# Performance work log

Measured on AMD Instinct MI355X. Metric: run time of the kernel, lower is better.

## Reference

```python
import jax, jax.numpy as jnp
import numpy as np

N_NODES = 100000
N_EDGES = 3200000
F_IN = 256
N_CLASSES = 10


def setup_inputs() -> dict:
    key = jax.random.key(0)
    ks = jax.random.split(key, 10)
    x = jax.random.normal(ks[0], (N_NODES, F_IN), dtype=jnp.float32)
    edge_index = jax.random.randint(ks[1], (2, N_EDGES), 0, N_NODES, dtype=jnp.int64)
    def glorot(k, fan_in, fan_out):
        s = (6.0 / (fan_in + fan_out)) ** 0.5
        return jax.random.uniform(k, (fan_in, fan_out), jnp.float32, -s, s)
    return {
        "x": x,
        "edge_index": edge_index,
        "W_gcn": glorot(ks[2], F_IN, 64),
        "b_gcn": jnp.zeros((64,), jnp.float32),
        "W1": glorot(ks[3], 64, 32),
        "b1": jnp.zeros((32,), jnp.float32),
        "W2": glorot(ks[4], 32, 16),
        "b2": jnp.zeros((16,), jnp.float32),
        "W3": glorot(ks[5], 16, N_CLASSES),
        "b3": jnp.zeros((N_CLASSES,), jnp.float32),
    }


def gcn_conv(x, edge_index, W, b):
    # PyG GCNConv: x' = D^{-1/2} (A + I) D^{-1/2} (x W) + b, with self-loops.
    n = x.shape[0]
    loop = jnp.arange(n, dtype=edge_index.dtype)
    src = jnp.concatenate([edge_index[0], loop])  # [E+N]
    dst = jnp.concatenate([edge_index[1], loop])
    deg = jax.ops.segment_sum(jnp.ones(src.shape, jnp.float32), dst, num_segments=n)
    dinv = jnp.where(deg > 0, jax.lax.rsqrt(deg), 0.0)
    norm = dinv[src] * dinv[dst]  # [E+N]
    h = x @ W  # transform first (reduces message width to 64)
    msg = h[src] * norm[:, None]  # gather + scale
    out = jax.ops.segment_sum(msg, dst, num_segments=n)  # scatter-add
    return out + b


def reference(x, edge_index, W_gcn, b_gcn, W1, b1, W2, b2, W3, b3):
    # Dropout is a no-op in eval mode; reference uses deterministic eval math.
    h = jax.nn.relu(gcn_conv(x, edge_index, W_gcn, b_gcn))
    h = jax.nn.relu(h @ W1 + b1)
    h = jax.nn.relu(h @ W2 + b2)
    return h @ W3 + b3
```

## Files before the change

### kernel.cpp

```cpp
#include <hip/hip_runtime.h>

#define F_IN 256
#define CHUNK 8192
#define CAP 10240

typedef short bf8_t __attribute__((ext_vector_type(8)));
typedef float f4_t  __attribute__((ext_vector_type(4)));

__device__ __forceinline__ unsigned short f2bf(float f) {
  unsigned u = __float_as_uint(f);
  unsigned r = (u + 0x7FFFu + ((u >> 16) & 1u)) >> 16;
  return (unsigned short)r;
}
#define BF_LO(d) __uint_as_float((d) << 16)
#define BF_HI(d) __uint_as_float((d) & 0xFFFF0000u)

__device__ __forceinline__ bf8_t pack8(float4 a, float4 b) {
  bf8_t r;
  r[0] = (short)f2bf(a.x); r[1] = (short)f2bf(a.y);
  r[2] = (short)f2bf(a.z); r[3] = (short)f2bf(a.w);
  r[4] = (short)f2bf(b.x); r[5] = (short)f2bf(b.y);
  r[6] = (short)f2bf(b.z); r[7] = (short)f2bf(b.w);
  return r;
}

__global__ __launch_bounds__(256) void wprep_kernel(
    const float* __restrict__ W, unsigned short* __restrict__ WbT) {
  const int i = blockIdx.x * 256 + threadIdx.x;
  const int k = i >> 6, n = i & 63;
  WbT[n * 256 + k] = f2bf(W[i]);
}

__global__ __launch_bounds__(256) void gemm_direct_kernel(
    const float* __restrict__ x, const unsigned short* __restrict__ WbT,
    const int* __restrict__ deg, unsigned short* __restrict__ hb, int M) {
  __shared__ short Bs[64][264];
  const int t = threadIdx.x;
  for (int i = t; i < 2048; i += 256) {
    const int n = i >> 5, kq = (i & 31) << 3;
    *(uint4*)&Bs[n][kq] = *(const uint4*)(WbT + n * 256 + kq);
  }
  __syncthreads();

  const int brow = blockIdx.x * 128;
  const int w = t >> 6;
  const int l = t & 63;
  const int ml = l & 15;
  const int quad = l >> 4;

  const int r0 = min(brow + w * 32 + ml, M - 1);
  const int r1 = min(brow + w * 32 + 16 + ml, M - 1);
  const float* xr0 = x + (size_t)r0 * F_IN + (quad << 3);
  const float* xr1 = x + (size_t)r1 * F_IN + (quad << 3);

  f4_t acc[2][4];
#pragma unroll
  for (int a = 0; a < 2; ++a)
#pragma unroll
    for (int b = 0; b < 4; ++b) acc[a][b] = (f4_t){0.f, 0.f, 0.f, 0.f};

#pragma unroll
  for (int k0 = 0; k0 < F_IN; k0 += 32) {
    bf8_t afr[2];
    {
      const float4 a0 = *(const float4*)(xr0 + k0);
      const float4 a1 = *(const float4*)(xr0 + k0 + 4);
      afr[0] = pack8(a0, a1);
      const float4 c0 = *(const float4*)(xr1 + k0);
      const float4 c1 = *(const float4*)(xr1 + k0 + 4);
      afr[1] = pack8(c0, c1);
    }
    bf8_t bfr[4];
#pragma unroll
    for (int nt = 0; nt < 4; ++nt)
      bfr[nt] = *(const bf8_t*)&Bs[nt * 16 + ml][k0 + (quad << 3)];
#pragma unroll
    for (int mt = 0; mt < 2; ++mt)
#pragma unroll
      for (int nt = 0; nt < 4; ++nt)
        acc[mt][nt] = __builtin_amdgcn_mfma_f32_16x16x32_bf16(
            afr[mt], bfr[nt], acc[mt][nt], 0, 0, 0);
  }

#pragma unroll
  for (int mt = 0; mt < 2; ++mt) {
#pragma unroll
    for (int reg = 0; reg < 4; ++reg) {
      const int row = brow + w * 32 + mt * 16 + (quad << 2) + reg;
      if (row < M) {
        const float di = rsqrtf((float)deg[row] + 1.f);
#pragma unroll
        for (int nt = 0; nt < 4; ++nt)
          hb[(size_t)row * 64 + nt * 16 + ml] = f2bf(di * acc[mt][nt][reg]);
      }
    }
  }
}

__global__ __launch_bounds__(512) void sort_local_kernel(
    const int* __restrict__ src_arr, const int* __restrict__ dst_arr,
    int* __restrict__ espB, int* __restrict__ segStart, int* __restrict__ segCnt,
    int E, int NBK) {
  __shared__ int hist[512];
  __shared__ int s[512];
  __shared__ int cur[512];
  const int t = threadIdx.x;
  const int blk = blockIdx.x;
  const int base = blk * CHUNK;
  const int cnt = min(CHUNK, E - base);
  for (int i = t; i < NBK; i += 512) hist[i] = 0;
  __syncthreads();
  int pk[16], bk[16];
#pragma unroll
  for (int k = 0; k < 16; ++k) {
    const int i = t + k * 512;
    bk[k] = -1;
    if (i < cnt) {
      const int sv = src_arr[base + i];
      const int dv = dst_arr[base + i];
      pk[k] = sv | ((dv & 255) << 24);
      bk[k] = dv >> 8;
      atomicAdd(&hist[bk[k]], 1);
    }
  }
  __syncthreads();
  const int v = (t < NBK) ? hist[t] : 0;
  s[t] = v;
  __syncthreads();
#pragma unroll
  for (int off = 1; off < 512; off <<= 1) {
    int add = (t >= off) ? s[t - off] : 0;
    __syncthreads();
    s[t] += add;
    __syncthreads();
  }
  if (t < NBK) {
    const int excl = s[t] - v;
    cur[t] = excl;
    segStart[blk * NBK + t] = base + excl;
    segCnt[blk * NBK + t] = v;
  }
  __syncthreads();
#pragma unroll
  for (int k = 0; k < 16; ++k) {
    if (bk[k] >= 0) {
      const int pos = atomicAdd(&cur[bk[k]], 1);
      espB[base + pos] = pk[k];
    }
  }
}

__global__ __launch_bounds__(512) void deg_hist_kernel(
    const int* __restrict__ espB, const int* __restrict__ segStart,
    const int* __restrict__ segCnt, int* __restrict__ deg,
    int N, int NBK, int NCH) {
  __shared__ int segS[512];
  __shared__ int segC[512];
  __shared__ int hist[256];
  const int t = threadIdx.x;
  const int b = blockIdx.x;
  segS[t] = 0;
  segC[t] = 0;
  if (t < 256) hist[t] = 0;
  __syncthreads();
  for (int i = t; i < NCH; i += 512) {
    segS[i] = segStart[i * NBK + b];
    segC[i] = segCnt[i * NBK + b];
  }
  __syncthreads();
  const int sw = t >> 4, sl = t & 15;
  for (int seg = sw; seg < NCH; seg += 32) {
    const int sS = segS[seg], c = segC[seg];
    for (int j = sl; j < c; j += 16)
      atomicAdd(&hist[((unsigned)espB[sS + j]) >> 24], 1);
  }
  __syncthreads();
  if (t < 256) {
    const int node = b * 256 + t;
    if (node < N) deg[node] = hist[t];
  }
}

__global__ __launch_bounds__(512) void bin_agg_kernel(
    const int* __restrict__ espB, const int* __restrict__ segStart,
    const int* __restrict__ segCnt, const int* __restrict__ deg,
    const unsigned short* __restrict__ hb, const float* __restrict__ bg,
    unsigned short* __restrict__ g, int N, int NBK, int NCH) {
  __shared__ int eLDS[CAP];
  __shared__ int segS[512];
  __shared__ int segC[512];
  __shared__ int sbuf[512];
  __shared__ int hist[256];
  __shared__ int cur[256];
  __shared__ int stt[256];
  const int t = threadIdx.x;
  const int b = blockIdx.x;
  segS[t] = 0;
  segC[t] = 0;
  __syncthreads();
  for (int i = t; i < NCH; i += 512) {
    segS[i] = segStart[i * NBK + b];
    segC[i] = segCnt[i * NBK + b];
  }
  int v2 = 0;
  if (t < 256) {
    const int node = b * 256 + t;
    v2 = (node < N) ? deg[node] : 0;
    sbuf[t] = v2;
  }
  __syncthreads();
#pragma unroll
  for (int off = 1; off < 256; off <<= 1) {
    int add = 0;
    if (t < 256 && t >= off) add = sbuf[t - off];
    __syncthreads();
    if (t < 256) sbuf[t] += add;
    __syncthreads();
  }
  if (t < 256) {
    const int excl = sbuf[t] - v2;
    cur[t] = excl;
    stt[t] = excl;
    hist[t] = v2;
  }
  __syncthreads();

  const int sw = t >> 4;
  const int sl = t & 15;

  for (int seg = sw; seg < NCH; seg += 32) {
    const int sS = segS[seg], c = segC[seg];
    for (int j = sl; j < c; j += 16) {
      const int p = espB[sS + j];
      const int pos = atomicAdd(&cur[((unsigned)p) >> 24], 1);
      if (pos < CAP) eLDS[pos] = p & 0x00FFFFFF;
    }
  }
  __syncthreads();

  const int w = t >> 6;
  const int lane = t & 63;
  const int slot = lane >> 3;
  const int fq = (lane & 7) << 3;

  for (int nn = 0; nn < 32; ++nn) {
    const int ln = w * 32 + nn;
    const int node = b * 256 + ln;
    const int cn = hist[ln];
    const int start = stt[ln];
    const int end = start + cn;

    float acc[8] = {0.f};
    if (cn > 0) {
      const int R = (cn + 31) >> 5;
      const int last = end - 1;
      int i = start + slot;
      int s0 = eLDS[min(i, last)];
      int s1 = eLDS[min(i + 8, last)];
      int s2 = eLDS[min(i + 16, last)];
      int s3 = eLDS[min(i + 24, last)];
      for (int r = 0; r < R; ++r) {
        const int i0 = i, i1 = i + 8, i2 = i + 16, i3 = i + 24;
        const uint4 r0 = *(const uint4*)(hb + (size_t)s0 * 64 + fq);
        const uint4 r1 = *(const uint4*)(hb + (size_t)s1 * 64 + fq);
        const uint4 r2 = *(const uint4*)(hb + (size_t)s2 * 64 + fq);
        const uint4 r3 = *(const uint4*)(hb + (size_t)s3 * 64 + fq);
        i += 32;
        if (r + 1 < R) {
          s0 = eLDS[min(i, last)];
          s1 = eLDS[min(i + 8, last)];
          s2 = eLDS[min(i + 16, last)];
          s3 = eLDS[min(i + 24, last)];
        }
        const float w0 = (i0 < end) ? 1.f : 0.f;
        const float w1 = (i1 < end) ? 1.f : 0.f;
        const float w2 = (i2 < end) ? 1.f : 0.f;
        const float w3 = (i3 < end) ? 1.f : 0.f;
        acc[0] = fmaf(w0, BF_LO(r0.x), acc[0]);
        acc[1] = fmaf(w0, BF_HI(r0.x), acc[1]);
        acc[2] = fmaf(w0, BF_LO(r0.y), acc[2]);
        acc[3] = fmaf(w0, BF_HI(r0.y), acc[3]);
        acc[4] = fmaf(w0, BF_LO(r0.z), acc[4]);
        acc[5] = fmaf(w0, BF_HI(r0.z), acc[5]);
        acc[6] = fmaf(w0, BF_LO(r0.w), acc[6]);
        acc[7] = fmaf(w0, BF_HI(r0.w), acc[7]);
        acc[0] = fmaf(w1, BF_LO(r1.x), acc[0]);
        acc[1] = fmaf(w1, BF_HI(r1.x), acc[1]);
        acc[2] = fmaf(w1, BF_LO(r1.y), acc[2]);
        acc[3] = fmaf(w1, BF_HI(r1.y), acc[3]);
        acc[4] = fmaf(w1, BF_LO(r1.z), acc[4]);
        acc[5] = fmaf(w1, BF_HI(r1.z), acc[5]);
        acc[6] = fmaf(w1, BF_LO(r1.w), acc[6]);
        acc[7] = fmaf(w1, BF_HI(r1.w), acc[7]);
        acc[0] = fmaf(w2, BF_LO(r2.x), acc[0]);
        acc[1] = fmaf(w2, BF_HI(r2.x), acc[1]);
        acc[2] = fmaf(w2, BF_LO(r2.y), acc[2]);
        acc[3] = fmaf(w2, BF_HI(r2.y), acc[3]);
        acc[4] = fmaf(w2, BF_LO(r2.z), acc[4]);
        acc[5] = fmaf(w2, BF_HI(r2.z), acc[5]);
        acc[6] = fmaf(w2, BF_LO(r2.w), acc[6]);
        acc[7] = fmaf(w2, BF_HI(r2.w), acc[7]);
        acc[0] = fmaf(w3, BF_LO(r3.x), acc[0]);
        acc[1] = fmaf(w3, BF_HI(r3.x), acc[1]);
        acc[2] = fmaf(w3, BF_LO(r3.y), acc[2]);
        acc[3] = fmaf(w3, BF_HI(r3.y), acc[3]);
        acc[4] = fmaf(w3, BF_LO(r3.z), acc[4]);
        acc[5] = fmaf(w3, BF_HI(r3.z), acc[5]);
        acc[6] = fmaf(w3, BF_LO(r3.w), acc[6]);
        acc[7] = fmaf(w3, BF_HI(r3.w), acc[7]);
      }
    }
#pragma unroll
    for (int m = 8; m <= 32; m <<= 1)
#pragma unroll
      for (int j = 0; j < 8; ++j) acc[j] += __shfl_xor(acc[j], m, 64);

    if (slot == 0 && node < N) {
      const float di = rsqrtf((float)(cn + 1));
      const uint4 r = *(const uint4*)(hb + (size_t)node * 64 + fq);
      const float4 bq0 = *(const float4*)(bg + fq);
      const float4 bq1 = *(const float4*)(bg + fq + 4);
      float4 v0 = make_float4(
          fmaxf(di * (acc[0] + BF_LO(r.x)) + bq0.x, 0.f),
          fmaxf(di * (acc[1] + BF_HI(r.x)) + bq0.y, 0.f),
          fmaxf(di * (acc[2] + BF_LO(r.y)) + bq0.z, 0.f),
          fmaxf(di * (acc[3] + BF_HI(r.y)) + bq0.w, 0.f));
      float4 v1 = make_float4(
          fmaxf(di * (acc[4] + BF_LO(r.z)) + bq1.x, 0.f),
          fmaxf(di * (acc[5] + BF_HI(r.z)) + bq1.y, 0.f),
          fmaxf(di * (acc[6] + BF_LO(r.w)) + bq1.z, 0.f),
          fmaxf(di * (acc[7] + BF_HI(r.w)) + bq1.w, 0.f));
      *(bf8_t*)(g + (size_t)node * 64 + fq) = pack8(v0, v1);
    }
  }
}

__global__ __launch_bounds__(256) void mlp_mfma_kernel(
    const unsigned short* __restrict__ g,
    const float* __restrict__ W1, const float* __restrict__ b1,
    const float* __restrict__ W2, const float* __restrict__ b2,
    const float* __restrict__ W3, const float* __restrict__ b3,
    float* __restrict__ out, int N) {
  __shared__ short g64[256 * 72];
  __shared__ short h2s[256 * 40];
  __shared__ short W1s[32 * 72];
  __shared__ short W2s[16 * 40];
  __shared__ short W3s[16 * 40];
  __shared__ float b1s[32], b2s[16], b3s[16];
  short* h1s = g64;

  const int t = threadIdx.x;
  const int node0 = blockIdx.x * 256;
  for (int i = t; i < 256 * 40; i += 256) h2s[i] = 0;
  for (int i = t; i < 16 * 40; i += 256) W3s[i] = 0;
  if (t < 32) b1s[t] = b1[t];
  if (t < 16) { b2s[t] = b2[t]; b3s[t] = (t < 10) ? b3[t] : 0.f; }
  __syncthreads();
  for (int i = t; i < 2048; i += 256) { const int k = i >> 5, n = i & 31; W1s[n * 72 + k] = (short)f2bf(W1[i]); }
  for (int i = t; i < 512;  i += 256) { const int k = i >> 4, n = i & 15; W2s[n * 40 + k] = (short)f2bf(W2[i]); }
  if (t < 160) { const int k = t / 10, n = t % 10; W3s[n * 40 + k] = (short)f2bf(W3[t]); }
  for (int i = t; i < 2048; i += 256) {
    const int row = i >> 3, q = (i & 7) << 3;
    const int nd = min(node0 + row, N - 1);
    *(uint4*)&g64[row * 72 + q] = *(const uint4*)(g + (size_t)nd * 64 + q);
  }
  __syncthreads();

  const int w = t >> 6;
  const int lane = t & 63;
  const int ml = lane & 15;
  const int quad = lane >> 4;

  bf8_t a1f[4][2], b1f[2][2];
#pragma unroll
  for (int mt = 0; mt < 4; ++mt)
#pragma unroll
    for (int ks = 0; ks < 2; ++ks)
      a1f[mt][ks] = *(const bf8_t*)&g64[(w * 64 + mt * 16 + ml) * 72 + ks * 32 + quad * 8];
#pragma unroll
  for (int nt = 0; nt < 2; ++nt)
#pragma unroll
    for (int ks = 0; ks < 2; ++ks)
      b1f[nt][ks] = *(const bf8_t*)&W1s[(nt * 16 + ml) * 72 + ks * 32 + quad * 8];
  f4_t acc1[4][2];
#pragma unroll
  for (int mt = 0; mt < 4; ++mt)
#pragma unroll
    for (int nt = 0; nt < 2; ++nt) acc1[mt][nt] = (f4_t){0.f, 0.f, 0.f, 0.f};
#pragma unroll
  for (int ks = 0; ks < 2; ++ks)
#pragma unroll
    for (int mt = 0; mt < 4; ++mt)
#pragma unroll
      for (int nt = 0; nt < 2; ++nt)
        acc1[mt][nt] = __builtin_amdgcn_mfma_f32_16x16x32_bf16(
            a1f[mt][ks], b1f[nt][ks], acc1[mt][nt], 0, 0, 0);
  __syncthreads();
#pragma unroll
  for (int mt = 0; mt < 4; ++mt)
#pragma unroll
    for (int nt = 0; nt < 2; ++nt)
#pragma unroll
      for (int reg = 0; reg < 4; ++reg) {
        const int row = w * 64 + mt * 16 + quad * 4 + reg;
        const int col = nt * 16 + ml;
        h1s[row * 40 + col] = (short)f2bf(fmaxf(acc1[mt][nt][reg] + b1s[col], 0.f));
      }
  __syncthreads();

  bf8_t a2f[4];
#pragma unroll
  for (int mt = 0; mt < 4; ++mt)
    a2f[mt] = *(const bf8_t*)&h1s[(w * 64 + mt * 16 + ml) * 40 + quad * 8];
  const bf8_t b2f = *(const bf8_t*)&W2s[ml * 40 + quad * 8];
  f4_t acc2[4];
#pragma unroll
  for (int mt = 0; mt < 4; ++mt) {
    acc2[mt] = (f4_t){0.f, 0.f, 0.f, 0.f};
    acc2[mt] = __builtin_amdgcn_mfma_f32_16x16x32_bf16(a2f[mt], b2f, acc2[mt], 0, 0, 0);
  }
  __syncthreads();
#pragma unroll
  for (int mt = 0; mt < 4; ++mt)
#pragma unroll
    for (int reg = 0; reg < 4; ++reg) {
      const int row = w * 64 + mt * 16 + quad * 4 + reg;
      h2s[row * 40 + ml] = (short)f2bf(fmaxf(acc2[mt][reg] + b2s[ml], 0.f));
    }
  __syncthreads();

  bf8_t a3f[4];
#pragma unroll
  for (int mt = 0; mt < 4; ++mt)
    a3f[mt] = *(const bf8_t*)&h2s[(w * 64 + mt * 16 + ml) * 40 + quad * 8];
  const bf8_t b3f = *(const bf8_t*)&W3s[ml * 40 + quad * 8];
#pragma unroll
  for (int mt = 0; mt < 4; ++mt) {
    f4_t acc3 = (f4_t){0.f, 0.f, 0.f, 0.f};
    acc3 = __builtin_amdgcn_mfma_f32_16x16x32_bf16(a3f[mt], b3f, acc3, 0, 0, 0);
#pragma unroll
    for (int reg = 0; reg < 4; ++reg) {
      const int node = node0 + w * 64 + mt * 16 + quad * 4 + reg;
      if (ml < 10 && node < N) out[(size_t)node * 10 + ml] = acc3[reg] + b3s[ml];
    }
  }
}

extern "C" void kernel_launch(void* const* d_in, const int* in_sizes, int n_in,
                              void* d_out, int out_size, void* d_ws, size_t ws_size,
                              hipStream_t stream) {
  const float* x     = (const float*)d_in[0];
  const int*   ei    = (const int*)d_in[1];
  const float* W_gcn = (const float*)d_in[2];
  const float* b_gcn = (const float*)d_in[3];
  const float* W1    = (const float*)d_in[4];
  const float* b1    = (const float*)d_in[5];
  const float* W2    = (const float*)d_in[6];
  const float* b2    = (const float*)d_in[7];
  const float* W3    = (const float*)d_in[8];
  const float* b3    = (const float*)d_in[9];
  float* out = (float*)d_out;

  const int N = in_sizes[0] / F_IN;
  const int E = in_sizes[1] / 2;
  const int* src = ei;
  const int* dst = ei + E;
  const int NBK = (N + 255) >> 8;
  const int NCH = (E + CHUNK - 1) / CHUNK;

  unsigned short* hb = (unsigned short*)d_ws;
  int*   deg         = (int*)(hb + (size_t)N * 64);
  int*   espB        = deg + N;
  int*   segStart    = espB + E;
  int*   segCnt      = segStart + NCH * NBK;
  unsigned short* WbT= (unsigned short*)(segCnt + NCH * NBK);
  unsigned short* g  = WbT + 16384;

  wprep_kernel<<<64, 256, 0, stream>>>(W_gcn, WbT);
  sort_local_kernel<<<NCH, 512, 0, stream>>>(
      src, dst, espB, segStart, segCnt, E, NBK);
  deg_hist_kernel<<<NBK, 512, 0, stream>>>(
      espB, segStart, segCnt, deg, N, NBK, NCH);

  gemm_direct_kernel<<<(N + 127) / 128, 256, 0, stream>>>(x, WbT, deg, hb, N);

  bin_agg_kernel<<<NBK, 512, 0, stream>>>(
      espB, segStart, segCnt, deg, hb, b_gcn, g, N, NBK, NCH);

  mlp_mfma_kernel<<<(N + 255) / 256, 256, 0, stream>>>(
      g, W1, b1, W2, b2, W3, b3, out, N);
}
```

Baseline: 322.3 us.

## Assign one 8-lane group per node in aggregation with padded zero-row sentinel

The gather-aggregate loop now gives each 8-lane group its own destination node, so a wave handles eight nodes at once instead of all 64 lanes working on one node and then reducing with cross-lane shuffles. Each node's edge list in LDS is padded to a multiple of four and filled with a sentinel index pointing at an extra zeroed row of h. This removes bounds masks, the FMA weights and the shuffle reductions. The trade-off is more load imbalance between nodes of different degree within a wave, plus an extra padding pass and a larger LDS footprint.

New measurement: 300.3 us (median of 2 runs). 6.8% less time.

```diff
diff --git a/kernel.cpp b/kernel.cpp
--- a/kernel.cpp
+++ b/kernel.cpp
@@ -25,10 +25,13 @@
 }
 
 __global__ __launch_bounds__(256) void wprep_kernel(
-    const float* __restrict__ W, unsigned short* __restrict__ WbT) {
-  const int i = blockIdx.x * 256 + threadIdx.x;
+    const float* __restrict__ W, unsigned short* __restrict__ WbT,
+    unsigned short* __restrict__ hb, int N) {
+  const int t = threadIdx.x;
+  const int i = blockIdx.x * 256 + t;
   const int k = i >> 6, n = i & 63;
   WbT[n * 256 + k] = f2bf(W[i]);
+  if (blockIdx.x == 0 && t < 64) hb[(size_t)N * 64 + t] = 0;
 }
 
 __global__ __launch_bounds__(256) void gemm_direct_kernel(
@@ -189,7 +192,7 @@
   __shared__ int eLDS[CAP];
   __shared__ int segS[512];
   __shared__ int segC[512];
-  __shared__ int sbuf[512];
+  __shared__ int sbuf[256];
   __shared__ int hist[256];
   __shared__ int cur[256];
   __shared__ int stt[256];
@@ -202,11 +205,12 @@
     segS[i] = segStart[i * NBK + b];
     segC[i] = segCnt[i * NBK + b];
   }
-  int v2 = 0;
+  int v2 = 0, vp = 0;
   if (t < 256) {
     const int node = b * 256 + t;
     v2 = (node < N) ? deg[node] : 0;
-    sbuf[t] = v2;
+    vp = (v2 + 3) & ~3;
+    sbuf[t] = vp;
   }
   __syncthreads();
 #pragma unroll
@@ -218,7 +222,7 @@
     __syncthreads();
   }
   if (t < 256) {
-    const int excl = sbuf[t] - v2;
+    const int excl = sbuf[t] - vp;
     cur[t] = excl;
     stt[t] = excl;
     hist[t] = v2;
@@ -237,99 +241,62 @@
     }
   }
   __syncthreads();
+  if (t < 256) {
+    const int e0 = cur[t];
+    const int e1 = stt[t] + ((hist[t] + 3) & ~3);
+    for (int i2 = e0; i2 < e1 && i2 < CAP; ++i2) eLDS[i2] = N;
+  }
+  __syncthreads();
 
   const int w = t >> 6;
   const int lane = t & 63;
-  const int slot = lane >> 3;
+  const int gi = lane >> 3;
   const int fq = (lane & 7) << 3;
 
-  for (int nn = 0; nn < 32; ++nn) {
-    const int ln = w * 32 + nn;
+#pragma unroll
+  for (int p = 0; p < 4; ++p) {
+    const int ln = p * 64 + w * 8 + gi;
     const int node = b * 256 + ln;
     const int cn = hist[ln];
     const int start = stt[ln];
-    const int end = start + cn;
-
-    float acc[8] = {0.f};
-    if (cn > 0) {
-      const int R = (cn + 31) >> 5;
-      const int last = end - 1;
-      int i = start + slot;
-      int s0 = eLDS[min(i, last)];
-      int s1 = eLDS[min(i + 8, last)];
-      int s2 = eLDS[min(i + 16, last)];
-      int s3 = eLDS[min(i + 24, last)];
-      for (int r = 0; r < R; ++r) {
-        const int i0 = i, i1 = i + 8, i2 = i + 16, i3 = i + 24;
-        const uint4 r0 = *(const uint4*)(hb + (size_t)s0 * 64 + fq);
-        const uint4 r1 = *(const uint4*)(hb + (size_t)s1 * 64 + fq);
-        const uint4 r2 = *(const uint4*)(hb + (size_t)s2 * 64 + fq);
-        const uint4 r3 = *(const uint4*)(hb + (size_t)s3 * 64 + fq);
-        i += 32;
-        if (r + 1 < R) {
-          s0 = eLDS[min(i, last)];
-          s1 = eLDS[min(i + 8, last)];
-          s2 = eLDS[min(i + 16, last)];
-          s3 = eLDS[min(i + 24, last)];
-        }
-        const float w0 = (i0 < end) ? 1.f : 0.f;
-        const float w1 = (i1 < end) ? 1.f : 0.f;
-        const float w2 = (i2 < end) ? 1.f : 0.f;
-        const float w3 = (i3 < end) ? 1.f : 0.f;
-        acc[0] = fmaf(w0, BF_LO(r0.x), acc[0]);
-        acc[1] = fmaf(w0, BF_HI(r0.x), acc[1]);
-        acc[2] = fmaf(w0, BF_LO(r0.y), acc[2]);
-        acc[3] = fmaf(w0, BF_HI(r0.y), acc[3]);
-        acc[4] = fmaf(w0, BF_LO(r0.z), acc[4]);
-        acc[5] = fmaf(w0, BF_HI(r0.z), acc[5]);
-        acc[6] = fmaf(w0, BF_LO(r0.w), acc[6]);
-        acc[7] = fmaf(w0, BF_HI(r0.w), acc[7]);
-        acc[0] = fmaf(w1, BF_LO(r1.x), acc[0]);
-        acc[1] = fmaf(w1, BF_HI(r1.x), acc[1]);
-        acc[2] = fmaf(w1, BF_LO(r1.y), acc[2]);
-        acc[3] = fmaf(w1, BF_HI(r1.y), acc[3]);
-        acc[4] = fmaf(w1, BF_LO(r1.z), acc[4]);
-        acc[5] = fmaf(w1, BF_HI(r1.z), acc[5]);
-        acc[6] = fmaf(w1, BF_LO(r1.w), acc[6]);
-        acc[7] = fmaf(w1, BF_HI(r1.w), acc[7]);
-        acc[0] = fmaf(w2, BF_LO(r2.x), acc[0]);
-        acc[1] = fmaf(w2, BF_HI(r2.x), acc[1]);
-        acc[2] = fmaf(w2, BF_LO(r2.y), acc[2]);
-        acc[3] = fmaf(w2, BF_HI(r2.y), acc[3]);
-        acc[4] = fmaf(w2, BF_LO(r2.z), acc[4]);
-        acc[5] = fmaf(w2, BF_HI(r2.z), acc[5]);
-        acc[6] = fmaf(w2, BF_LO(r2.w), acc[6]);
-        acc[7] = fmaf(w2, BF_HI(r2.w), acc[7]);
-        acc[0] = fmaf(w3, BF_LO(r3.x), acc[0]);
-        acc[1] = fmaf(w3, BF_HI(r3.x), acc[1]);
-        acc[2] = fmaf(w3, BF_LO(r3.y), acc[2]);
-        acc[3] = fmaf(w3, BF_HI(r3.y), acc[3]);
-        acc[4] = fmaf(w3, BF_LO(r3.z), acc[4]);
-        acc[5] = fmaf(w3, BF_HI(r3.z), acc[5]);
-        acc[6] = fmaf(w3, BF_LO(r3.w), acc[6]);
-        acc[7] = fmaf(w3, BF_HI(r3.w), acc[7]);
-      }
-    }
-#pragma unroll
-    for (int m = 8; m <= 32; m <<= 1)
-#pragma unroll
-      for (int j = 0; j < 8; ++j) acc[j] += __shfl_xor(acc[j], m, 64);
-
-    if (slot == 0 && node < N) {
+    const int R = (cn + 3) >> 2;
+
+    float acc[8] = {0.f, 0.f, 0.f, 0.f, 0.f, 0.f, 0.f, 0.f};
+    int i = start;
+    int s0 = 0, s1 = 0, s2 = 0, s3 = 0;
+    if (R > 0) { s0 = eLDS[i]; s1 = eLDS[i + 1]; s2 = eLDS[i + 2]; s3 = eLDS[i + 3]; }
+    for (int r = 0; r < R; ++r) {
+      const uint4 r0 = *(const uint4*)(hb + (size_t)s0 * 64 + fq);
+      const uint4 r1 = *(const uint4*)(hb + (size_t)s1 * 64 + fq);
+      const uint4 r2 = *(const uint4*)(hb + (size_t)s2 * 64 + fq);
+      const uint4 r3 = *(const uint4*)(hb + (size_t)s3 * 64 + fq);
+      i += 4;
+      if (r + 1 < R) { s0 = eLDS[i]; s1 = eLDS[i + 1]; s2 = eLDS[i + 2]; s3 = eLDS[i + 3]; }
+      acc[0] += (BF_LO(r0.x) + BF_LO(r1.x)) + (BF_LO(r2.x) + BF_LO(r3.x));
+      acc[1] += (BF_HI(r0.x) + BF_HI(r1.x)) + (BF_HI(r2.x) + BF_HI(r3.x));
+      acc[2] += (BF_LO(r0.y) + BF_LO(r1.y)) + (BF_LO(r2.y) + BF_LO(r3.y));
+      acc[3] += (BF_HI(r0.y) + BF_HI(r1.y)) + (BF_HI(r2.y) + BF_HI(r3.y));
+      acc[4] += (BF_LO(r0.z) + BF_LO(r1.z)) + (BF_LO(r2.z) + BF_LO(r3.z));
+      acc[5] += (BF_HI(r0.z) + BF_HI(r1.z)) + (BF_HI(r2.z) + BF_HI(r3.z));
+      acc[6] += (BF_LO(r0.w) + BF_LO(r1.w)) + (BF_LO(r2.w) + BF_LO(r3.w));
+      acc[7] += (BF_HI(r0.w) + BF_HI(r1.w)) + (BF_HI(r2.w) + BF_HI(r3.w));
+    }
+
+    if (node < N) {
       const float di = rsqrtf((float)(cn + 1));
-      const uint4 r = *(const uint4*)(hb + (size_t)node * 64 + fq);
+      const uint4 rr = *(const uint4*)(hb + (size_t)node * 64 + fq);
       const float4 bq0 = *(const float4*)(bg + fq);
       const float4 bq1 = *(const float4*)(bg + fq + 4);
       float4 v0 = make_float4(
-          fmaxf(di * (acc[0] + BF_LO(r.x)) + bq0.x, 0.f),
-          fmaxf(di * (acc[1] + BF_HI(r.x)) + bq0.y, 0.f),
-          fmaxf(di * (acc[2] + BF_LO(r.y)) + bq0.z, 0.f),
-          fmaxf(di * (acc[3] + BF_HI(r.y)) + bq0.w, 0.f));
+          fmaxf(di * (acc[0] + BF_LO(rr.x)) + bq0.x, 0.f),
+          fmaxf(di * (acc[1] + BF_HI(rr.x)) + bq0.y, 0.f),
+          fmaxf(di * (acc[2] + BF_LO(rr.y)) + bq0.z, 0.f),
+          fmaxf(di * (acc[3] + BF_HI(rr.y)) + bq0.w, 0.f));
       float4 v1 = make_float4(
-          fmaxf(di * (acc[4] + BF_LO(r.z)) + bq1.x, 0.f),
-          fmaxf(di * (acc[5] + BF_HI(r.z)) + bq1.y, 0.f),
-          fmaxf(di * (acc[6] + BF_LO(r.w)) + bq1.z, 0.f),
-          fmaxf(di * (acc[7] + BF_HI(r.w)) + bq1.w, 0.f));
+          fmaxf(di * (acc[4] + BF_LO(rr.z)) + bq1.x, 0.f),
+          fmaxf(di * (acc[5] + BF_HI(rr.z)) + bq1.y, 0.f),
+          fmaxf(di * (acc[6] + BF_LO(rr.w)) + bq1.z, 0.f),
+          fmaxf(di * (acc[7] + BF_HI(rr.w)) + bq1.w, 0.f));
       *(bf8_t*)(g + (size_t)node * 64 + fq) = pack8(v0, v1);
     }
   }
@@ -469,14 +436,14 @@
   const int NCH = (E + CHUNK - 1) / CHUNK;
 
   unsigned short* hb = (unsigned short*)d_ws;
-  int*   deg         = (int*)(hb + (size_t)N * 64);
+  int*   deg         = (int*)(hb + (size_t)(N + 1) * 64);
   int*   espB        = deg + N;
   int*   segStart    = espB + E;
   int*   segCnt      = segStart + NCH * NBK;
   unsigned short* WbT= (unsigned short*)(segCnt + NCH * NBK);
   unsigned short* g  = WbT + 16384;
 
-  wprep_kernel<<<64, 256, 0, stream>>>(W_gcn, WbT);
+  wprep_kernel<<<64, 256, 0, stream>>>(W_gcn, WbT, hb, N);
   sort_local_kernel<<<NCH, 512, 0, stream>>>(
       src, dst, espB, segStart, segCnt, E, NBK);
   deg_hist_kernel<<<NBK, 512, 0, stream>>>(
```
